# Kernel tuning notes

Measured on AMD Instinct MI355X. Metric: run time of the kernel, lower is better.

Reference implementation:

```python
import jax, jax.numpy as jnp
import numpy as np
import math

EMBED_DIM = 1024
N_HEADS = 16
QK_DIM = 64
V_DIM = 64
B, S = 4, 2048


def setup_inputs() -> dict:
    key = jax.random.key(0)
    ks = jax.random.split(key, 10)
    sc = lambda fan_in: 1.0 / math.sqrt(fan_in)
    X = jax.random.normal(ks[0], (B, S, EMBED_DIM), dtype=jnp.float32)
    mask = jax.random.randint(ks[1], (B, 1, S, S), 0, 2, dtype=jnp.int32)
    wQ = jax.random.uniform(ks[2], (EMBED_DIM, QK_DIM * N_HEADS), jnp.float32, -sc(EMBED_DIM), sc(EMBED_DIM))
    bQ = jnp.zeros((QK_DIM * N_HEADS,), jnp.float32)
    wK = jax.random.uniform(ks[3], (EMBED_DIM, QK_DIM * N_HEADS), jnp.float32, -sc(EMBED_DIM), sc(EMBED_DIM))
    bK = jnp.zeros((QK_DIM * N_HEADS,), jnp.float32)
    wV = jax.random.uniform(ks[4], (EMBED_DIM, V_DIM * N_HEADS), jnp.float32, -sc(EMBED_DIM), sc(EMBED_DIM))
    bV = jnp.zeros((V_DIM * N_HEADS,), jnp.float32)
    wO = jax.random.uniform(ks[5], (V_DIM * N_HEADS, EMBED_DIM), jnp.float32, -sc(V_DIM * N_HEADS), sc(V_DIM * N_HEADS))
    bO = jnp.zeros((EMBED_DIM,), jnp.float32)
    return {"X": X, "mask": mask, "wQ": wQ, "bQ": bQ, "wK": wK, "bK": bK,
            "wV": wV, "bV": bV, "wO": wO, "bO": bO}


def reference(X, mask, wQ, bQ, wK, bK, wV, bV, wO, bO):
    Bsz, Slen, _ = X.shape
    # projections -> [B, H, S, d]
    q = (X @ wQ + bQ).reshape(Bsz, Slen, N_HEADS, QK_DIM).transpose(0, 2, 1, 3)
    k = (X @ wK + bK).reshape(Bsz, Slen, N_HEADS, QK_DIM).transpose(0, 2, 1, 3)
    v = (X @ wV + bV).reshape(Bsz, Slen, N_HEADS, V_DIM).transpose(0, 2, 1, 3)
    # scores [B, H, S, S]
    scores = jnp.einsum("bhqd,bhkd->bhqk", q, k) / math.sqrt(QK_DIM)
    scores = jnp.where(mask == 0, jnp.float32(-1e9), scores)
    probs = jax.nn.softmax(scores, axis=-1)
    out = jnp.einsum("bhqk,bhkd->bhqd", probs, v)  # [B, H, S, v]
    out = out.transpose(0, 2, 1, 3).reshape(Bsz, Slen, N_HEADS * V_DIM)
    return out @ wO + bO
```

## Files before the change

### kernel.cpp

```cpp
#include <hip/hip_runtime.h>
#include <hip/hip_bf16.h>

#define EMB 1024
#define NH 16
#define DH 64
#define SEQ 2048

typedef __attribute__((ext_vector_type(8))) __bf16 bf16x8;
typedef __attribute__((ext_vector_type(4))) float f32x4;

__device__ __forceinline__ void g2l16(const void* g, void* l) {
  __builtin_amdgcn_global_load_lds(
      (const __attribute__((address_space(1))) void*)g,
      (__attribute__((address_space(3))) void*)l, 16, 0, 0);
}

__global__ void detect_k(const unsigned short* __restrict__ xs,
                         int* __restrict__ flag) {
  __shared__ int cnt;
  if (threadIdx.x == 0) cnt = 0;
  __syncthreads();
  int hits = 0;
  for (int i = threadIdx.x; i < 16384; i += 256) {
    unsigned e = (xs[i] >> 7) & 0xFFu;
    if (e >= 0xC0u) hits++;
  }
  atomicAdd(&cnt, hits);
  __syncthreads();
  if (threadIdx.x == 0) *flag = (cnt > 16) ? 1 : 0;
}

__global__ void conv_k(const void* __restrict__ src,
                       __hip_bfloat16* __restrict__ dst,
                       const int* __restrict__ flag, int n4) {
  int i = blockIdx.x * 256 + threadIdx.x;
  if (i >= n4) return;
  if (*flag) {
    float4 v = ((const float4*)src)[i];
    ushort4 o;
    __hip_bfloat16 t;
    t = __float2bfloat16(v.x); o.x = *(unsigned short*)&t;
    t = __float2bfloat16(v.y); o.y = *(unsigned short*)&t;
    t = __float2bfloat16(v.z); o.z = *(unsigned short*)&t;
    t = __float2bfloat16(v.w); o.w = *(unsigned short*)&t;
    ((ushort4*)dst)[i] = o;
  } else {
    ((ushort4*)dst)[i] = ((const ushort4*)src)[i];
  }
}

__global__ void convB_k(const void* s0, const void* s1, const void* s2,
                        const void* s3, __hip_bfloat16* __restrict__ dst,
                        const int* __restrict__ flag) {
  const void* srcs[4] = {s0, s1, s2, s3};
  const void* src = srcs[blockIdx.x];
  int i = threadIdx.x;
  __hip_bfloat16* d = dst + blockIdx.x * 1024;
  if (*flag) {
    float4 v = ((const float4*)src)[i];
    ushort4 o;
    __hip_bfloat16 t;
    t = __float2bfloat16(v.x); o.x = *(unsigned short*)&t;
    t = __float2bfloat16(v.y); o.y = *(unsigned short*)&t;
    t = __float2bfloat16(v.z); o.z = *(unsigned short*)&t;
    t = __float2bfloat16(v.w); o.w = *(unsigned short*)&t;
    ((ushort4*)d)[i] = o;
  } else {
    ((ushort4*)d)[i] = ((const ushort4*)src)[i];
  }
}

__global__ void transW4_k(const void* s0, const void* s1, const void* s2,
                          const void* s3, __hip_bfloat16* d0,
                          __hip_bfloat16* d1, __hip_bfloat16* d2,
                          __hip_bfloat16* d3, const int* __restrict__ flag) {
  __shared__ __hip_bfloat16 tile[32][33];
  const void* srcs[4] = {s0, s1, s2, s3};
  __hip_bfloat16* dsts[4] = {d0, d1, d2, d3};
  const void* src = srcs[blockIdx.z];
  __hip_bfloat16* dst = dsts[blockIdx.z];
  int f = *flag;
  int tx = threadIdx.x, ty = threadIdx.y;
  int x = blockIdx.x * 32 + tx;
  int y0 = blockIdx.y * 32;
  for (int i = 0; i < 32; i += 8) {
    int idx = (y0 + ty + i) * EMB + x;
    tile[ty + i][tx] = f ? __float2bfloat16(((const float*)src)[idx])
                         : ((const __hip_bfloat16*)src)[idx];
  }
  __syncthreads();
  int x2 = y0 + tx;
  int y2 = blockIdx.x * 32;
  for (int i = 0; i < 32; i += 8)
    dst[(size_t)(y2 + ty + i) * EMB + x2] = tile[tx][ty + i];
}

__global__ void maskpack_k(const int* __restrict__ mask,
                           unsigned int* __restrict__ bits) {
  int g = blockIdx.x * 256 + threadIdx.x;
  int lane = threadIdx.x & 63;
  unsigned long long bal = __ballot(mask[g] != 0);
  if ((lane & 31) == 0)
    bits[g >> 5] = (unsigned int)(bal >> (lane & 32));
}

__launch_bounds__(256)
__global__ void gemm_qkv(const __hip_bfloat16* __restrict__ A,
                         const __hip_bfloat16* __restrict__ Bt,
                         const __hip_bfloat16* __restrict__ bias,
                         __hip_bfloat16* __restrict__ CQ,
                         __hip_bfloat16* __restrict__ CK,
                         __hip_bfloat16* __restrict__ CV) {
  __shared__ __align__(16) __bf16 sA[128 * 32];
  __shared__ __align__(16) __bf16 sB[128 * 32];
  const __bf16* Ab = (const __bf16*)A;
  const __bf16* Bb = (const __bf16*)Bt;

  int tid = threadIdx.x;
  int w = tid >> 6, lane = tid & 63;
  int quad = lane >> 4, lcol = lane & 15;
  int m0 = blockIdx.x * 128, n0 = blockIdx.y * 128;
  int wm = (w >> 1) * 64, wn = (w & 1) * 64;
  int region = n0 >> 10;

  f32x4 z = {0.f, 0.f, 0.f, 0.f};
  f32x4 acc[4][4];
#pragma unroll
  for (int i = 0; i < 4; i++)
#pragma unroll
    for (int j = 0; j < 4; j++) acc[i][j] = z;

  int c = w * 64 + lane;
  int r = c >> 2, cc = c & 3;

  for (int k0 = 0; k0 < 1024; k0 += 32) {
    __syncthreads();
    g2l16(Ab + (size_t)(m0 + r) * 1024 + k0 + cc * 8, (char*)sA + w * 1024);
    g2l16(Ab + (size_t)(m0 + r + 64) * 1024 + k0 + cc * 8, (char*)sA + 4096 + w * 1024);
    g2l16(Bb + (size_t)(n0 + r) * 1024 + k0 + cc * 8, (char*)sB + w * 1024);
    g2l16(Bb + (size_t)(n0 + r + 64) * 1024 + k0 + cc * 8, (char*)sB + 4096 + w * 1024);
    __syncthreads();

    bf16x8 af[4], bfr[4];
#pragma unroll
    for (int i = 0; i < 4; i++)
      af[i] = *(const bf16x8*)(sA + (wm + i * 16 + lcol) * 32 + quad * 8);
#pragma unroll
    for (int j = 0; j < 4; j++)
      bfr[j] = *(const bf16x8*)(sB + (wn + j * 16 + lcol) * 32 + quad * 8);
#pragma unroll
    for (int i = 0; i < 4; i++)
#pragma unroll
      for (int j = 0; j < 4; j++)
        acc[i][j] = __builtin_amdgcn_mfma_f32_16x16x32_bf16(af[i], bfr[j], acc[i][j], 0, 0, 0);
  }

  float scale = (region == 0) ? 0.18033688011111204f : 1.0f;
#pragma unroll
  for (int j = 0; j < 4; j++) {
    int col = n0 + wn + j * 16 + lcol;
    float bv = __bfloat162float(bias[col]);
    int lc = col & 1023;
    int h = lc >> 6, dd = lc & 63;
#pragma unroll
    for (int i = 0; i < 4; i++) {
      int rbase = m0 + wm + i * 16 + quad * 4;
#pragma unroll
      for (int rr = 0; rr < 4; rr++) {
        int m = rbase + rr;
        int b = m >> 11, s = m & 2047;
        float v = (acc[i][j][rr] + bv) * scale;
        __hip_bfloat16 hv = __float2bfloat16(v);
        if (region == 0)
          CQ[(((size_t)(b * NH + h)) * SEQ + s) * DH + dd] = hv;
        else if (region == 1)
          CK[(((size_t)(b * NH + h)) * SEQ + s) * DH + dd] = hv;
        else
          CV[(((size_t)(b * NH + h)) * DH + dd) * SEQ + s] = hv;
      }
    }
  }
}

__launch_bounds__(256)
__global__ void gemm_o(const __hip_bfloat16* __restrict__ A,
                       const __hip_bfloat16* __restrict__ Bt,
                       const __hip_bfloat16* __restrict__ bias,
                       void* __restrict__ Cv, const int* __restrict__ flag) {
  __shared__ __align__(16) __bf16 sA[128 * 32];
  __shared__ __align__(16) __bf16 sB[128 * 32];
  const __bf16* Ab = (const __bf16*)A;
  const __bf16* Bb = (const __bf16*)Bt;
  int f32out = *flag;

  int tid = threadIdx.x;
  int w = tid >> 6, lane = tid & 63;
  int quad = lane >> 4, lcol = lane & 15;
  int m0 = blockIdx.x * 128, n0 = blockIdx.y * 128;
  int wm = (w >> 1) * 64, wn = (w & 1) * 64;

  f32x4 z = {0.f, 0.f, 0.f, 0.f};
  f32x4 acc[4][4];
#pragma unroll
  for (int i = 0; i < 4; i++)
#pragma unroll
    for (int j = 0; j < 4; j++) acc[i][j] = z;

  int c = w * 64 + lane;
  int r = c >> 2, cc = c & 3;

  for (int k0 = 0; k0 < 1024; k0 += 32) {
    __syncthreads();
    g2l16(Ab + (size_t)(m0 + r) * 1024 + k0 + cc * 8, (char*)sA + w * 1024);
    g2l16(Ab + (size_t)(m0 + r + 64) * 1024 + k0 + cc * 8, (char*)sA + 4096 + w * 1024);
    g2l16(Bb + (size_t)(n0 + r) * 1024 + k0 + cc * 8, (char*)sB + w * 1024);
    g2l16(Bb + (size_t)(n0 + r + 64) * 1024 + k0 + cc * 8, (char*)sB + 4096 + w * 1024);
    __syncthreads();

    bf16x8 af[4], bfr[4];
#pragma unroll
    for (int i = 0; i < 4; i++)
      af[i] = *(const bf16x8*)(sA + (wm + i * 16 + lcol) * 32 + quad * 8);
#pragma unroll
    for (int j = 0; j < 4; j++)
      bfr[j] = *(const bf16x8*)(sB + (wn + j * 16 + lcol) * 32 + quad * 8);
#pragma unroll
    for (int i = 0; i < 4; i++)
#pragma unroll
      for (int j = 0; j < 4; j++)
        acc[i][j] = __builtin_amdgcn_mfma_f32_16x16x32_bf16(af[i], bfr[j], acc[i][j], 0, 0, 0);
  }

#pragma unroll
  for (int j = 0; j < 4; j++) {
    int col = n0 + wn + j * 16 + lcol;
    float bv = __bfloat162float(bias[col]);
#pragma unroll
    for (int i = 0; i < 4; i++) {
      int rbase = m0 + wm + i * 16 + quad * 4;
#pragma unroll
      for (int rr = 0; rr < 4; rr++) {
        int m = rbase + rr;
        float v = acc[i][j][rr] + bv;
        if (f32out)
          ((float*)Cv)[(size_t)m * EMB + col] = v;
        else
          ((__hip_bfloat16*)Cv)[(size_t)m * EMB + col] = __float2bfloat16(v);
      }
    }
  }
}

__launch_bounds__(256)
__global__ void attn_k(const __hip_bfloat16* __restrict__ Qp,
                       const __hip_bfloat16* __restrict__ Kp,
                       const __hip_bfloat16* __restrict__ Vp,
                       const unsigned int* __restrict__ mbits,
                       __hip_bfloat16* __restrict__ AO) {
  __shared__ __align__(16) __bf16 sK[64 * 64];
  __shared__ __align__(16) __bf16 sV[64 * 64];
  __shared__ __align__(16) __bf16 sP[4 * 16 * 72];
  __shared__ unsigned long long sLut[16];

  int tid = threadIdx.x;
  int w = tid >> 6, lane = tid & 63, quad = lane >> 4, lcol = lane & 15;
  int qblk = blockIdx.x;
  int bh = blockIdx.y;
  int b = bh >> 4, h = bh & 15;

  if (tid < 16) {
    unsigned long long v = 0;
    if (tid & 1) v |= 0xFFFFull;
    if (tid & 2) v |= 0xFFFFull << 16;
    if (tid & 4) v |= 0xFFFFull << 32;
    if (tid & 8) v |= 0xFFFFull << 48;
    sLut[tid] = v;
  }

  const __bf16* Qb = (const __bf16*)Qp + (size_t)bh * SEQ * DH;
  const __bf16* Kb = (const __bf16*)Kp + (size_t)bh * SEQ * DH;
  const __bf16* Vb = (const __bf16*)Vp + (size_t)bh * DH * SEQ;
  int qw = qblk * 64 + w * 16;
  int q_mine = qw + lcol;

  bf16x8 bq0 = *(const bf16x8*)(Qb + (size_t)q_mine * DH + quad * 8);
  bf16x8 bq1 = *(const bf16x8*)(Qb + (size_t)q_mine * DH + 32 + quad * 8);

  __bf16 onev = (__bf16)1.0f;
  bf16x8 ones = {onev, onev, onev, onev, onev, onev, onev, onev};

  f32x4 z = {0.f, 0.f, 0.f, 0.f};
  f32x4 ot[4];
  f32x4 lacc = z;
#pragma unroll
  for (int j = 0; j < 4; j++) ot[j] = z;

  const unsigned long long* mrow =
      (const unsigned long long*)mbits + ((size_t)b * SEQ + q_mine) * (SEQ / 64);

  int kr = lane >> 3, pc = lane & 7;
  __bf16* pw = sP + w * (16 * 72);

  for (int kt = 0; kt < SEQ / 64; ++kt) {
    __syncthreads();
#pragma unroll
    for (int t2 = 0; t2 < 2; t2++) {
      int row = w * 16 + t2 * 8 + kr;
      g2l16(Kb + (size_t)(kt * 64 + row) * DH + (pc ^ kr) * 8,
            (char*)sK + (w * 16 + t2 * 8) * 128);
      g2l16(Vb + (size_t)row * SEQ + kt * 64 + (pc ^ kr) * 8,
            (char*)sV + (w * 16 + t2 * 8) * 128);
    }
    __syncthreads();

    f32x4 st[4];
    int swz = lcol & 7;
#pragma unroll
    for (int t = 0; t < 4; t++) {
      int rowK = t * 16 + lcol;
      bf16x8 a0 = *(const bf16x8*)(sK + rowK * 64 + (quad ^ swz) * 8);
      bf16x8 a1 = *(const bf16x8*)(sK + rowK * 64 + ((quad + 4) ^ swz) * 8);
      f32x4 sv = __builtin_amdgcn_mfma_f32_16x16x32_bf16(a0, bq0, z, 0, 0, 0);
      sv = __builtin_amdgcn_mfma_f32_16x16x32_bf16(a1, bq1, sv, 0, 0, 0);
      st[t] = sv;
    }

    unsigned long long mb64 = mrow[kt];
    unsigned int lo32 = (unsigned int)(mb64 >> (quad * 4));
    unsigned int hi32 = (unsigned int)(mb64 >> (quad * 4 + 32));
#pragma unroll
    for (int t = 0; t < 4; t++) {
      unsigned int sel = (t < 2) ? lo32 : hi32;
      unsigned int bits4 = (sel >> ((t & 1) * 16)) & 0xFu;
      union { unsigned long long u; __bf16 bb[4]; } pk;
#pragma unroll
      for (int r = 0; r < 4; r++)
        pk.bb[r] = (__bf16)__builtin_amdgcn_exp2f(st[t][r]);
      pk.u &= sLut[bits4];
      *(unsigned long long*)(pw + lcol * 72 + t * 16 + quad * 4) = pk.u;
    }

    bf16x8 bp0 = *(const bf16x8*)(pw + lcol * 72 + quad * 8);
    bf16x8 bp1 = *(const bf16x8*)(pw + lcol * 72 + 32 + quad * 8);
#pragma unroll
    for (int j = 0; j < 4; j++) {
      int rowV = j * 16 + lcol;
      bf16x8 av0 = *(const bf16x8*)(sV + rowV * 64 + (quad ^ swz) * 8);
      bf16x8 av1 = *(const bf16x8*)(sV + rowV * 64 + ((quad + 4) ^ swz) * 8);
      ot[j] = __builtin_amdgcn_mfma_f32_16x16x32_bf16(av0, bp0, ot[j], 0, 0, 0);
      ot[j] = __builtin_amdgcn_mfma_f32_16x16x32_bf16(av1, bp1, ot[j], 0, 0, 0);
    }
    lacc = __builtin_amdgcn_mfma_f32_16x16x32_bf16(ones, bp0, lacc, 0, 0, 0);
    lacc = __builtin_amdgcn_mfma_f32_16x16x32_bf16(ones, bp1, lacc, 0, 0, 0);
  }

  float linv = 1.0f / fmaxf(lacc[0], 1e-20f);
#pragma unroll
  for (int j = 0; j < 4; j++) {
    union { ushort4 u; __bf16 bb[4]; } pk;
#pragma unroll
    for (int r = 0; r < 4; r++) pk.bb[r] = (__bf16)(ot[j][r] * linv);
    *(ushort4*)((__bf16*)AO + ((size_t)b * SEQ + q_mine) * EMB + h * 64 +
                j * 16 + quad * 4) = pk.u;
  }
}

extern "C" void kernel_launch(void* const* d_in, const int* in_sizes, int n_in,
                              void* d_out, int out_size, void* d_ws, size_t ws_size,
                              hipStream_t stream) {
  const int* mask = (const int*)d_in[1];

  char* ws = (char*)d_ws;
  int* flag             = (int*)ws;
  __hip_bfloat16* biasc = (__hip_bfloat16*)(ws + (64ull << 10));
  __hip_bfloat16* WQt   = (__hip_bfloat16*)(ws + (1ull << 20));
  __hip_bfloat16* WKt   = (__hip_bfloat16*)(ws + (3ull << 20));
  __hip_bfloat16* WVt   = (__hip_bfloat16*)(ws + (5ull << 20));
  __hip_bfloat16* WOt   = (__hip_bfloat16*)(ws + (7ull << 20));
  unsigned int* mbits   = (unsigned int*)(ws + (9ull << 20));
  __hip_bfloat16* Xc    = (__hip_bfloat16*)(ws + (12ull << 20));
  __hip_bfloat16* Qw    = (__hip_bfloat16*)(ws + (28ull << 20));
  __hip_bfloat16* Kw    = (__hip_bfloat16*)(ws + (44ull << 20));
  __hip_bfloat16* Vtw   = (__hip_bfloat16*)(ws + (60ull << 20));
  __hip_bfloat16* AO    = (__hip_bfloat16*)(ws + (76ull << 20));

  detect_k<<<1, 256, 0, stream>>>((const unsigned short*)d_in[0], flag);

  conv_k<<<8192, 256, 0, stream>>>(d_in[0], Xc, flag, 2097152);
  convB_k<<<4, 256, 0, stream>>>(d_in[3], d_in[5], d_in[7], d_in[9], biasc, flag);

  dim3 tb(32, 8);
  transW4_k<<<dim3(32, 32, 4), tb, 0, stream>>>(d_in[2], d_in[4], d_in[6],
                                                d_in[8], WQt, WKt, WVt, WOt, flag);
  maskpack_k<<<65536, 256, 0, stream>>>(mask, mbits);

  gemm_qkv<<<dim3(64, 24), 256, 0, stream>>>(Xc, WQt, biasc, Qw, Kw, Vtw);
  attn_k<<<dim3(32, 64), 256, 0, stream>>>(Qw, Kw, Vtw, mbits, AO);
  gemm_o<<<dim3(64, 8), 256, 0, stream>>>(AO, WOt, biasc + 3072, d_out, flag);
}
```

Baseline: 426.0 us.

## Store Q transposed with packed writes and remap attention blocks per XCD

The QKV projection epilogue now writes Q in the same transposed [d][seq] layout as V, using packed 8-byte stores of four consecutive rows instead of scalar strided stores. The attention kernel gathers Q from that transposed layout. Block IDs are remapped so that blocks sharing a batch-head land on the same XCD, which should improve L2 reuse of K/V. The exp2 input is clamped at 80 to avoid overflow, and the Q reads in attention become strided scalar gathers.

```diff
diff --git a/kernel.cpp b/kernel.cpp
--- a/kernel.cpp
+++ b/kernel.cpp
@@ -165,18 +165,20 @@
 #pragma unroll
     for (int i = 0; i < 4; i++) {
       int rbase = m0 + wm + i * 16 + quad * 4;
-#pragma unroll
-      for (int rr = 0; rr < 4; rr++) {
-        int m = rbase + rr;
-        int b = m >> 11, s = m & 2047;
-        float v = (acc[i][j][rr] + bv) * scale;
-        __hip_bfloat16 hv = __float2bfloat16(v);
-        if (region == 0)
-          CQ[(((size_t)(b * NH + h)) * SEQ + s) * DH + dd] = hv;
-        else if (region == 1)
-          CK[(((size_t)(b * NH + h)) * SEQ + s) * DH + dd] = hv;
-        else
-          CV[(((size_t)(b * NH + h)) * DH + dd) * SEQ + s] = hv;
+      int b = rbase >> 11, s = rbase & 2047;
+      if (region == 1) {
+#pragma unroll
+        for (int rr = 0; rr < 4; rr++) {
+          float v = acc[i][j][rr] + bv;
+          CK[(((size_t)(b * NH + h)) * SEQ + s + rr) * DH + dd] = __float2bfloat16(v);
+        }
+      } else {
+        union { unsigned long long u; __hip_bfloat16 bb[4]; } pk;
+#pragma unroll
+        for (int rr = 0; rr < 4; rr++)
+          pk.bb[rr] = __float2bfloat16((acc[i][j][rr] + bv) * scale);
+        __hip_bfloat16* dst = (region == 0) ? CQ : CV;
+        *(unsigned long long*)(dst + (((size_t)(b * NH + h)) * DH + dd) * SEQ + s) = pk.u;
       }
     }
   }
@@ -252,7 +254,7 @@
 }
 
 __launch_bounds__(256)
-__global__ void attn_k(const __hip_bfloat16* __restrict__ Qp,
+__global__ void attn_k(const __hip_bfloat16* __restrict__ Qt,
                        const __hip_bfloat16* __restrict__ Kp,
                        const __hip_bfloat16* __restrict__ Vp,
                        const unsigned int* __restrict__ mbits,
@@ -264,8 +266,10 @@
 
   int tid = threadIdx.x;
   int w = tid >> 6, lane = tid & 63, quad = lane >> 4, lcol = lane & 15;
-  int qblk = blockIdx.x;
-  int bh = blockIdx.y;
+  int bid = blockIdx.y * 32 + blockIdx.x;
+  int xcd = bid & 7, idx = bid >> 3;
+  int bh = xcd * 8 + (idx >> 5);
+  int qblk = idx & 31;
   int b = bh >> 4, h = bh & 15;
 
   if (tid < 16) {
@@ -277,14 +281,19 @@
     sLut[tid] = v;
   }
 
-  const __bf16* Qb = (const __bf16*)Qp + (size_t)bh * SEQ * DH;
+  const __bf16* Qb = (const __bf16*)Qt + (size_t)bh * DH * SEQ;
   const __bf16* Kb = (const __bf16*)Kp + (size_t)bh * SEQ * DH;
   const __bf16* Vb = (const __bf16*)Vp + (size_t)bh * DH * SEQ;
   int qw = qblk * 64 + w * 16;
   int q_mine = qw + lcol;
 
-  bf16x8 bq0 = *(const bf16x8*)(Qb + (size_t)q_mine * DH + quad * 8);
-  bf16x8 bq1 = *(const bf16x8*)(Qb + (size_t)q_mine * DH + 32 + quad * 8);
+  union { bf16x8 v; __bf16 e[8]; } uq0, uq1;
+#pragma unroll
+  for (int j = 0; j < 8; j++) {
+    uq0.e[j] = Qb[(size_t)(quad * 8 + j) * SEQ + q_mine];
+    uq1.e[j] = Qb[(size_t)(32 + quad * 8 + j) * SEQ + q_mine];
+  }
+  bf16x8 bq0 = uq0.v, bq1 = uq1.v;
 
   __bf16 onev = (__bf16)1.0f;
   bf16x8 ones = {onev, onev, onev, onev, onev, onev, onev, onev};
@@ -335,7 +344,7 @@
       union { unsigned long long u; __bf16 bb[4]; } pk;
 #pragma unroll
       for (int r = 0; r < 4; r++)
-        pk.bb[r] = (__bf16)__builtin_amdgcn_exp2f(st[t][r]);
+        pk.bb[r] = (__bf16)__builtin_amdgcn_exp2f(fminf(st[t][r], 80.f));
       pk.u &= sLut[bits4];
       *(unsigned long long*)(pw + lcol * 72 + t * 16 + quad * 4) = pk.u;
     }
```

New measurement: 425.1 us. Within noise of the previous version (-0.2%).
